# Optimization experiments

Hardware: AMD Instinct MI355X
Metric: run time of the kernel (lower is better)

The kernel has to match this reference:

```python
import jax, jax.numpy as jnp
import numpy as np

D_MODEL = 1024
NUM_HEADS = 16
HEAD_SIZE = D_MODEL // NUM_HEADS  # 64; used ONLY as the softmax scale (module never splits heads)


def setup_inputs() -> dict:
    key = jax.random.key(0)
    ks = jax.random.split(key, 7)
    B, L, D = 4, 2048, D_MODEL
    q = jax.random.normal(ks[0], (B, L, D), dtype=jnp.float32)
    k = jax.random.normal(ks[1], (B, L, D), dtype=jnp.float32)
    v = jax.random.normal(ks[2], (B, L, D), dtype=jnp.float32)
    s = 1.0 / np.sqrt(D)
    Wq = jax.random.uniform(ks[3], (D, D), jnp.float32, -s, s)
    Wk = jax.random.uniform(ks[4], (D, D), jnp.float32, -s, s)
    Wv = jax.random.uniform(ks[5], (D, D), jnp.float32, -s, s)
    Wproj = jax.random.uniform(ks[6], (D, D), jnp.float32, -s, s)
    return {"q": q, "k": k, "v": v, "Wq": Wq, "Wk": Wk, "Wv": Wv, "Wproj": Wproj}


def reference(q, k, v, Wq, Wk, Wv, Wproj):
    # nn.Linear(x) = x @ W.T; weights stored [out, in]
    L = q.shape[1]
    qh = jnp.einsum('bld,ed->ble', q, Wq)
    kh = jnp.einsum('bld,ed->ble', k, Wk)
    vh = jnp.einsum('bld,ed->ble', v, Wv)
    # NOTE: module attends over the full d_model channel (no head split),
    # but scales by head_size ** -0.5 — faithful to the source.
    att = jnp.einsum('bqd,bkd->bqk', qh, kh) * (HEAD_SIZE ** -0.5)
    causal = jnp.tril(jnp.ones((L, L), dtype=bool))  # bias buffer
    att = jnp.where(causal, att, -jnp.inf)
    att = jax.nn.softmax(att, axis=-1)
    y = jnp.einsum('bqk,bkd->bqd', att, vh)
    y = jnp.einsum('bld,ed->ble', y, Wproj)
    return y
```

## Files before the change

kernel.cpp:

```cpp
#include <hip/hip_runtime.h>
#include <hip/hip_bf16.h>
#include <stdint.h>

typedef __bf16 bf16x8 __attribute__((ext_vector_type(8)));
typedef float  f32x4  __attribute__((ext_vector_type(4)));
typedef unsigned short ushort8v __attribute__((ext_vector_type(8)));

__device__ __forceinline__ unsigned short f2bf(float f) {
  unsigned int u = __float_as_uint(f);
  u += 0x7FFF + ((u >> 16) & 1);
  return (unsigned short)(u >> 16);
}
__device__ __forceinline__ float bf2f(unsigned short h) {
  return __uint_as_float(((unsigned int)h) << 16);
}

#define GLOAD_LDS(gptr, ldsptr)                                                     \
  __builtin_amdgcn_global_load_lds(                                                 \
      (const __attribute__((address_space(1))) unsigned int*)(gptr),                \
      (__attribute__((address_space(3))) unsigned int*)(ldsptr), 16, 0, 0)

__global__ __launch_bounds__(512, 1) void gemm8p(
    const unsigned short* __restrict__ A,
    const unsigned short* __restrict__ B,
    unsigned short* __restrict__ C,
    int M, int N, int K, int ntn)
{
  const int nwg = gridDim.x, orig = blockIdx.x;
  const int qq = nwg >> 3, rr = nwg & 7, xcd = orig & 7, oo = orig >> 3;
  const int wg = (xcd < rr ? xcd * (qq + 1) : rr * (qq + 1) + (xcd - rr) * qq) + oo;
  const int mt = wg / ntn, nt = wg % ntn;

  __shared__ __align__(16) unsigned short lds[65536];

  const int tid  = threadIdx.x;
  const int wave = tid >> 6;
  const int lane = tid & 63;
  const int wr = wave >> 2, wc = wave & 3;
  const int li = lane & 15;
  const int rslot = (((lane >> 4) ^ ((lane >> 1) & 3)) << 4);

  f32x4 acc[8][4];
#pragma unroll
  for (int i = 0; i < 8; ++i)
#pragma unroll
    for (int j = 0; j < 4; ++j) acc[i][j] = (f32x4){0.f, 0.f, 0.f, 0.f};

  const int nkt = K / 64;

  const int srow = tid >> 2;
  const long scol = (long)(((tid & 3) ^ ((tid >> 3) & 3)) << 3);
  const long aoff0 = (long)(mt * 256 + srow) * K + scol;
  const long aoff1 = (long)(mt * 256 + 128 + srow) * K + scol;
  const long boff0 = (long)(nt * 256 + srow) * K + scol;
  const long boff1 = (long)(nt * 256 + 128 + srow) * K + scol;
  const int stw = wave * 1024;

#define AB(c, kh) (((c) * 2 + (kh)) * 16384)
#define BB(c, kh) (65536 + ((c) * 2 + (kh)) * 16384)
#define STAGE_A(c, kh, jt) do { const long o_ = (long)(jt) * 64 + (kh) * 32;        \
    GLOAD_LDS(A + aoff0 + o_, (char*)lds + AB(c, kh) + stw);                        \
    GLOAD_LDS(A + aoff1 + o_, (char*)lds + AB(c, kh) + 8192 + stw); } while (0)
#define STAGE_B(c, kh, jt) do { const long o_ = (long)(jt) * 64 + (kh) * 32;        \
    GLOAD_LDS(B + boff0 + o_, (char*)lds + BB(c, kh) + stw);                        \
    GLOAD_LDS(B + boff1 + o_, (char*)lds + BB(c, kh) + 8192 + stw); } while (0)
#define RD_A(c, kk, ms, mf) \
  (*(const bf16x8*)((const char*)lds + AB(c, kk) + (wr * 128 + (ms) * 64 + (mf) * 16 + li) * 64 + rslot))
#define RD_B(c, kk, nf) \
  (*(const bf16x8*)((const char*)lds + BB(c, kk) + (wc * 64 + (nf) * 16 + li) * 64 + rslot))
#define MM(msb, bb) do {                                                            \
    _Pragma("unroll")                                                               \
    for (int mf_ = 0; mf_ < 4; ++mf_)                                               \
    _Pragma("unroll")                                                               \
      for (int nf_ = 0; nf_ < 4; ++nf_)                                             \
        acc[(msb) + mf_][nf_] = __builtin_amdgcn_mfma_f32_16x16x32_bf16(            \
            a[mf_], bb[nf_], acc[(msb) + mf_][nf_], 0, 0, 0); } while (0)
#define LGKM0_FENCE do {                                                            \
    asm volatile("s_waitcnt lgkmcnt(0)" ::: "memory");                              \
    __builtin_amdgcn_sched_barrier(0); } while (0)
#define BARRIER do { __builtin_amdgcn_s_barrier();                                  \
    asm volatile("" ::: "memory"); } while (0)

  STAGE_A(0, 0, 0); STAGE_B(0, 0, 0); STAGE_A(0, 1, 0); STAGE_B(0, 1, 0);
  asm volatile("s_waitcnt vmcnt(0)" ::: "memory");
  BARRIER;

  bf16x8 a[4], b0[4], b1[4];
  for (int j = 0; j < nkt; ++j) {
    const int c = j & 1;
    const bool more = (j + 1 < nkt);

#pragma unroll
    for (int nf = 0; nf < 4; ++nf) b0[nf] = RD_B(c, 0, nf);
#pragma unroll
    for (int mf = 0; mf < 4; ++mf) a[mf] = RD_A(c, 0, 0, mf);
    if (more) STAGE_A(c ^ 1, 0, j + 1);
    BARRIER;
    LGKM0_FENCE;
    __builtin_amdgcn_s_setprio(1);
    MM(0, b0);
    __builtin_amdgcn_s_setprio(0);
    BARRIER;

#pragma unroll
    for (int mf = 0; mf < 4; ++mf) a[mf] = RD_A(c, 0, 1, mf);
    if (more) STAGE_B(c ^ 1, 0, j + 1);
    BARRIER;
    LGKM0_FENCE;
    __builtin_amdgcn_s_setprio(1);
    MM(4, b0);
    __builtin_amdgcn_s_setprio(0);
    asm volatile("s_waitcnt vmcnt(4)" ::: "memory");
    BARRIER;

#pragma unroll
    for (int nf = 0; nf < 4; ++nf) b1[nf] = RD_B(c, 1, nf);
#pragma unroll
    for (int mf = 0; mf < 4; ++mf) a[mf] = RD_A(c, 1, 0, mf);
    if (more) STAGE_A(c ^ 1, 1, j + 1);
    BARRIER;
    LGKM0_FENCE;
    __builtin_amdgcn_s_setprio(1);
    MM(0, b1);
    __builtin_amdgcn_s_setprio(0);
    BARRIER;

#pragma unroll
    for (int mf = 0; mf < 4; ++mf) a[mf] = RD_A(c, 1, 1, mf);
    if (more) STAGE_B(c ^ 1, 1, j + 1);
    BARRIER;
    LGKM0_FENCE;
    __builtin_amdgcn_s_setprio(1);
    MM(4, b1);
    __builtin_amdgcn_s_setprio(0);
    asm volatile("s_waitcnt vmcnt(4)" ::: "memory");
    BARRIER;
  }
#undef AB
#undef BB
#undef STAGE_A
#undef STAGE_B
#undef RD_A
#undef RD_B
#undef MM
#undef LGKM0_FENCE
#undef BARRIER

  const int rb = mt * 256 + wr * 128;
  const int cb = nt * 256 + wc * 64;
#pragma unroll
  for (int mi = 0; mi < 8; ++mi)
#pragma unroll
    for (int ni = 0; ni < 4; ++ni) {
      const int row0 = rb + mi * 16 + ((lane >> 4) << 2);
      const int col  = cb + ni * 16 + (lane & 15);
#pragma unroll
      for (int jj = 0; jj < 4; ++jj)
        C[(long)(row0 + jj) * N + col] = f2bf(acc[mi][ni][jj]);
    }
}

#define BM 128
#define BN 128
#define BK 32

__global__ __launch_bounds__(256, 3) void gemm_bt(
    const unsigned short* __restrict__ A,
    const unsigned short* __restrict__ B,
    void* __restrict__ C,
    int M, int N, int K, int ntiles,
    long sAz, long sBz, long sCz,
    int mode, int tilemap, float scale)
{
  int mt, nt;
  const int orig = blockIdx.x;
  if (tilemap == 0) {
    const int nwg = gridDim.x;
    const int qq = nwg >> 3, rr = nwg & 7, xc = orig & 7, oo = orig >> 3;
    const int wg = (xc < rr ? xc * (qq + 1) : rr * (qq + 1) + (xc - rr) * qq) + oo;
    mt = wg / ntiles; nt = wg % ntiles;
  } else if (tilemap == 1) {
    mt = (int)((sqrtf(8.f * orig + 1.f) - 1.f) * 0.5f);
    int base = mt * (mt + 1) / 2;
    if (orig < base) { mt--; base = mt * (mt + 1) / 2; }
    else if (orig >= base + mt + 1) { mt++; base = mt * (mt + 1) / 2; }
    nt = orig - base;
  } else {
    const int c = orig & 15;
    mt = (c & 8) ? (15 - (c & 7)) : c;
    nt = orig >> 4;
  }
  const int z = blockIdx.y;
  const int emode = (mode == 3) ? (z == 2 ? 1 : 0) : mode;

  A += sAz * (long)z;
  B += sBz * (long)z;

  __shared__ __align__(16) unsigned short As[3][BM * BK];
  __shared__ __align__(16) unsigned short Bs[3][BN * BK];

  const int tid  = threadIdx.x;
  const int wave = tid >> 6;
  const int lane = tid & 63;
  const int wr = wave >> 1, wc = wave & 1;

  f32x4 acc[4][4];
#pragma unroll
  for (int i = 0; i < 4; ++i)
#pragma unroll
    for (int j = 0; j < 4; ++j) acc[i][j] = (f32x4){0.f, 0.f, 0.f, 0.f};

  int kiters = K / BK;
  if (tilemap == 2) { const int kl = (mt + 1) * (BM / BK); if (kl < kiters) kiters = kl; }

  const int r0 = tid >> 2, s0 = tid & 3;
  const int c0 = ((s0 ^ ((r0 >> 1) & 3)) << 3);
  const int r1 = r0 + 64;
  const int c1 = ((s0 ^ ((r1 >> 1) & 3)) << 3);
  const long aoff0 = (long)(mt * BM + r0) * K + c0;
  const long aoff1 = (long)(mt * BM + r1) * K + c1;
  const long boff0 = (long)(nt * BN + r0) * K + c0;
  const long boff1 = (long)(nt * BN + r1) * K + c1;
  const unsigned ldsw = wave * 1024;

#define STAGE(bi, k0)                                                     \
  do {                                                                    \
    GLOAD_LDS(A + aoff0 + (k0), (char*)&As[bi][0]    + ldsw);             \
    GLOAD_LDS(A + aoff1 + (k0), (char*)&As[bi][2048] + ldsw);             \
    GLOAD_LDS(B + boff0 + (k0), (char*)&Bs[bi][0]    + ldsw);             \
    GLOAD_LDS(B + boff1 + (k0), (char*)&Bs[bi][2048] + ldsw);             \
  } while (0)

  STAGE(0, 0);
  if (kiters > 1) STAGE(1, BK);

  int cur = 0;
  for (int kt = 0; kt < kiters; ++kt) {
    const int rem = kiters - 1 - kt;
    if (rem >= 2) {
      int sb = cur + 2; if (sb >= 3) sb -= 3;
      STAGE(sb, (kt + 2) * BK);
      asm volatile("s_waitcnt vmcnt(8)" ::: "memory");
    } else if (rem == 1) {
      asm volatile("s_waitcnt vmcnt(4)" ::: "memory");
    } else {
      asm volatile("s_waitcnt vmcnt(0)" ::: "memory");
    }
    __builtin_amdgcn_s_barrier();
    asm volatile("" ::: "memory");

    bf16x8 af[4], bfr[4];
#pragma unroll
    for (int i = 0; i < 4; ++i) {
      const int ar = wr * 64 + i * 16 + (lane & 15);
      const int as = ((lane >> 4) ^ ((ar >> 1) & 3)) << 3;
      af[i] = *(const bf16x8*)&As[cur][ar * BK + as];
      const int br = wc * 64 + i * 16 + (lane & 15);
      const int bs = ((lane >> 4) ^ ((br >> 1) & 3)) << 3;
      bfr[i] = *(const bf16x8*)&Bs[cur][br * BK + bs];
    }
#pragma unroll
    for (int mi = 0; mi < 4; ++mi)
#pragma unroll
      for (int ni = 0; ni < 4; ++ni)
        acc[mi][ni] = __builtin_amdgcn_mfma_f32_16x16x32_bf16(af[mi], bfr[ni], acc[mi][ni], 0, 0, 0);

    asm volatile("" ::: "memory");
    __builtin_amdgcn_s_barrier();
    cur = (cur == 2) ? 0 : cur + 1;
  }
#undef STAGE

  const int rb = mt * BM + wr * 64;
  const int cb = nt * BN + wc * 64;

  if (emode == 0) {
    unsigned short* Cb = (unsigned short*)C + sCz * (long)z;
#pragma unroll
    for (int mi = 0; mi < 4; ++mi)
#pragma unroll
      for (int ni = 0; ni < 4; ++ni) {
        const int row0 = rb + mi * 16 + ((lane >> 4) << 2);
        const int col  = cb + ni * 16 + (lane & 15);
#pragma unroll
        for (int j = 0; j < 4; ++j)
          Cb[(long)(row0 + j) * N + col] = f2bf(acc[mi][ni][j] * scale);
      }
  } else if (emode == 1) {
    unsigned short* Cb = (unsigned short*)C + sCz * (long)z;
#pragma unroll
    for (int mi = 0; mi < 4; ++mi)
#pragma unroll
      for (int ni = 0; ni < 4; ++ni) {
        const int row0 = rb + mi * 16 + ((lane >> 4) << 2);
        const int col  = cb + ni * 16 + (lane & 15);
#pragma unroll
        for (int j = 0; j < 4; ++j) {
          const int row = row0 + j;
          const int b = row >> 11, l = row & 2047;
          Cb[((long)b * N + col) * 2048 + l] = f2bf(acc[mi][ni][j]);
        }
      }
  } else {
    float* Cf = (float*)C + sCz * (long)z;
#pragma unroll
    for (int mi = 0; mi < 4; ++mi)
#pragma unroll
      for (int ni = 0; ni < 4; ++ni) {
        const int row0 = rb + mi * 16 + ((lane >> 4) << 2);
        const int col  = cb + ni * 16 + (lane & 15);
#pragma unroll
        for (int j = 0; j < 4; ++j)
          Cf[(long)(row0 + j) * N + col] = acc[mi][ni][j] * scale;
      }
  }
}

__global__ __launch_bounds__(256) void softmax_causal(
    const unsigned short* __restrict__ S, unsigned short* __restrict__ P)
{
  const int r = blockIdx.x;
  const int b = r >> 11, q = r & 2047;
  const unsigned short* srow = S + ((long)b * 2048 + q) * 2048;
  unsigned short* prow = P + ((long)b * 2048 + q) * 2048;
  const int len = q + 1;
  const int lenceil = ((q >> 7) + 1) << 7;
  const int tid = threadIdx.x, lane = tid & 63, wave = tid >> 6;
  const int base = tid * 8;
  const bool active = base < lenceil;
  __shared__ float red[8];

  float vv[8];
#pragma unroll
  for (int i = 0; i < 8; ++i) vv[i] = -3.4e38f;
  if (active) {
    ushort8v xv = *(const ushort8v*)(srow + base);
#pragma unroll
    for (int i = 0; i < 8; ++i) vv[i] = bf2f(xv[i]);
  }

  float m = -3.4e38f;
#pragma unroll
  for (int i = 0; i < 8; ++i) if (base + i < len) m = fmaxf(m, vv[i]);
#pragma unroll
  for (int o = 32; o; o >>= 1) m = fmaxf(m, __shfl_xor(m, o));
  if (lane == 0) red[wave] = m;
  __syncthreads();
  m = fmaxf(fmaxf(red[0], red[1]), fmaxf(red[2], red[3]));

  float p[8], s = 0.f;
#pragma unroll
  for (int i = 0; i < 8; ++i) {
    p[i] = (base + i < len) ? __expf(vv[i] - m) : 0.f;
    s += p[i];
  }
#pragma unroll
  for (int o = 32; o; o >>= 1) s += __shfl_xor(s, o);
  if (lane == 0) red[4 + wave] = s;
  __syncthreads();
  s = (red[4] + red[5]) + (red[6] + red[7]);
  const float inv = 1.f / s;

  if (active) {
    ushort8v o16;
#pragma unroll
    for (int i = 0; i < 8; ++i) o16[i] = f2bf(p[i] * inv);
    *(ushort8v*)(prow + base) = o16;
  }
}

__global__ __launch_bounds__(256) void convert_all(
    const float* __restrict__ q, const float* __restrict__ k, const float* __restrict__ v,
    const float* __restrict__ wq, const float* __restrict__ wk,
    const float* __restrict__ wv, const float* __restrict__ wp,
    unsigned short* __restrict__ qkv, unsigned short* __restrict__ wb)
{
  const long NQ = 8192L * 1024 / 4;
  const long NW = 1024L * 1024 / 4;
  const int blk = blockIdx.x;
  const float* src; unsigned short* dst; long n; int nb, bb;
  if (blk < 1536) {
    const int s = blk >> 9;
    src = (s == 0) ? q : (s == 1) ? k : v;
    dst = qkv + (long)s * (8192L * 1024);
    n = NQ; nb = 512; bb = blk & 511;
  } else {
    const int s = (blk - 1536) >> 6;
    src = (s == 0) ? wq : (s == 1) ? wk : (s == 2) ? wv : wp;
    dst = wb + (long)s * (1024L * 1024);
    n = NW; nb = 64; bb = (blk - 1536) & 63;
  }
  for (long i = (long)bb * 256 + threadIdx.x; i < n; i += (long)nb * 256) {
    float4 x = ((const float4*)src)[i];
    ushort4 o;
    o.x = f2bf(x.x); o.y = f2bf(x.y); o.z = f2bf(x.z); o.w = f2bf(x.w);
    ((ushort4*)dst)[i] = o;
  }
}

extern "C" void kernel_launch(void* const* d_in, const int* in_sizes, int n_in,
                              void* d_out, int out_size, void* d_ws, size_t ws_size,
                              hipStream_t stream) {
  const float* q  = (const float*)d_in[0];
  const float* k  = (const float*)d_in[1];
  const float* v  = (const float*)d_in[2];
  const float* Wq = (const float*)d_in[3];
  const float* Wk = (const float*)d_in[4];
  const float* Wv = (const float*)d_in[5];
  const float* Wp = (const float*)d_in[6];
  float* out = (float*)d_out;

  const long D  = 1024;
  const long L  = 2048;
  const long ND = 8192 * D;
  const long NS = 4L * L * L;

  char* ws = (char*)d_ws;
  unsigned short* qh    = (unsigned short*)ws;
  unsigned short* kh    = qh  + ND;
  unsigned short* vhT   = kh  + ND;
  unsigned short* wbf   = vhT + ND;
  unsigned short* S     = wbf + 4L * D * D;
  unsigned short* qkvbf = S   + NS;
  unsigned short* P     = qkvbf;
  unsigned short* ybf   = P + NS;

  convert_all<<<1792, 256, 0, stream>>>(q, k, v, Wq, Wk, Wv, Wp, qkvbf, wbf);

  gemm8p<<<128, 512, 0, stream>>>(qkvbf, wbf, S, 8192, 1024, 1024, 4);

  gemm_bt<<<dim3(512, 3), 256, 0, stream>>>(qkvbf, wbf, qh,
      8192, 1024, 1024, 8, ND, D * D, ND, 3, 0, 1.0f);

  gemm_bt<<<dim3(136, 4), 256, 0, stream>>>(qh, kh, S,
      2048, 2048, 1024, 16, L * D, L * D, L * L, 0, 1, 0.125f);

  softmax_causal<<<8192, 256, 0, stream>>>(S, P);

  gemm_bt<<<dim3(128, 4), 256, 0, stream>>>(P, vhT, ybf,
      2048, 1024, 2048, 8, L * L, D * L, L * D, 0, 2, 1.0f);

  gemm_bt<<<dim3(512, 1), 256, 0, stream>>>(ybf, wbf + 3 * D * D, out,
      8192, 1024, 1024, 8, 0, 0, 0, 2, 0, 1.0f);
}
```

Before: 250.2 us.

## Route QKV projection and causal QK^T through 256x256 deep-prefetch GEMM kernel

Generalizes the 512-thread 256x256-tile gemm8p kernel with batch strides, epilogue modes, scale and a triangular tile map. The QKV projection and the causal QK^T now run on it instead of the 128x128 gemm_bt kernel. It also drops a stray gemm8p warm-up launch that wrote into S. The kernel's LDS prefetch is deepened so the next k-half is staged earlier, with adjusted vmcnt waits, to hide global load latency. Larger tiles cut redundant operand traffic, but occupancy is lower and the triangular grid has only 36 tiles per batch, which leaves some CUs idle and adds tail imbalance.

```diff
diff --git a/kernel.cpp b/kernel.cpp
--- a/kernel.cpp
+++ b/kernel.cpp
@@ -23,13 +23,29 @@
 __global__ __launch_bounds__(512, 1) void gemm8p(
     const unsigned short* __restrict__ A,
     const unsigned short* __restrict__ B,
-    unsigned short* __restrict__ C,
-    int M, int N, int K, int ntn)
+    void* __restrict__ C,
+    int M, int N, int K, int ntn,
+    long sAz, long sBz, long sCz,
+    int mode, int tilemap, float scale)
 {
-  const int nwg = gridDim.x, orig = blockIdx.x;
-  const int qq = nwg >> 3, rr = nwg & 7, xcd = orig & 7, oo = orig >> 3;
-  const int wg = (xcd < rr ? xcd * (qq + 1) : rr * (qq + 1) + (xcd - rr) * qq) + oo;
-  const int mt = wg / ntn, nt = wg % ntn;
+  int mt, nt;
+  const int orig = blockIdx.x;
+  if (tilemap == 0) {
+    const int nwg = gridDim.x;
+    const int qq = nwg >> 3, rr = nwg & 7, xcd = orig & 7, oo = orig >> 3;
+    const int wg = (xcd < rr ? xcd * (qq + 1) : rr * (qq + 1) + (xcd - rr) * qq) + oo;
+    mt = wg / ntn; nt = wg % ntn;
+  } else {
+    mt = (int)((sqrtf(8.f * orig + 1.f) - 1.f) * 0.5f);
+    int base = mt * (mt + 1) / 2;
+    if (orig < base) { mt--; base = mt * (mt + 1) / 2; }
+    else if (orig >= base + mt + 1) { mt++; base = mt * (mt + 1) / 2; }
+    nt = orig - base;
+  }
+  const int z = blockIdx.y;
+  const int emode = (mode == 3) ? (z == 2 ? 1 : 0) : mode;
+  A += sAz * (long)z;
+  B += sBz * (long)z;
 
   __shared__ __align__(16) unsigned short lds[65536];
 
@@ -82,19 +98,22 @@
     asm volatile("" ::: "memory"); } while (0)
 
   STAGE_A(0, 0, 0); STAGE_B(0, 0, 0); STAGE_A(0, 1, 0); STAGE_B(0, 1, 0);
-  asm volatile("s_waitcnt vmcnt(0)" ::: "memory");
+  if (nkt > 1) { STAGE_A(1, 0, 1); STAGE_B(1, 0, 1); }
+  if (nkt > 1) { asm volatile("s_waitcnt vmcnt(4)" ::: "memory"); }
+  else         { asm volatile("s_waitcnt vmcnt(0)" ::: "memory"); }
   BARRIER;
 
   bf16x8 a[4], b0[4], b1[4];
   for (int j = 0; j < nkt; ++j) {
     const int c = j & 1;
-    const bool more = (j + 1 < nkt);
+    const bool s1 = (j + 1 < nkt);
+    const bool s2 = (j + 2 < nkt);
 
 #pragma unroll
     for (int nf = 0; nf < 4; ++nf) b0[nf] = RD_B(c, 0, nf);
 #pragma unroll
     for (int mf = 0; mf < 4; ++mf) a[mf] = RD_A(c, 0, 0, mf);
-    if (more) STAGE_A(c ^ 1, 0, j + 1);
+    if (s1) STAGE_A(c ^ 1, 1, j + 1);
     BARRIER;
     LGKM0_FENCE;
     __builtin_amdgcn_s_setprio(1);
@@ -104,20 +123,21 @@
 
 #pragma unroll
     for (int mf = 0; mf < 4; ++mf) a[mf] = RD_A(c, 0, 1, mf);
-    if (more) STAGE_B(c ^ 1, 0, j + 1);
+    if (s1) STAGE_B(c ^ 1, 1, j + 1);
     BARRIER;
     LGKM0_FENCE;
     __builtin_amdgcn_s_setprio(1);
     MM(4, b0);
     __builtin_amdgcn_s_setprio(0);
-    asm volatile("s_waitcnt vmcnt(4)" ::: "memory");
+    if (s1) { asm volatile("s_waitcnt vmcnt(8)" ::: "memory"); }
+    else    { asm volatile("s_waitcnt vmcnt(0)" ::: "memory"); }
     BARRIER;
 
 #pragma unroll
     for (int nf = 0; nf < 4; ++nf) b1[nf] = RD_B(c, 1, nf);
 #pragma unroll
     for (int mf = 0; mf < 4; ++mf) a[mf] = RD_A(c, 1, 0, mf);
-    if (more) STAGE_A(c ^ 1, 1, j + 1);
+    if (s2) STAGE_A(c, 0, j + 2);
     BARRIER;
     LGKM0_FENCE;
     __builtin_amdgcn_s_setprio(1);
@@ -127,13 +147,14 @@
 
 #pragma unroll
     for (int mf = 0; mf < 4; ++mf) a[mf] = RD_A(c, 1, 1, mf);
-    if (more) STAGE_B(c ^ 1, 1, j + 1);
+    if (s2) STAGE_B(c, 0, j + 2);
     BARRIER;
     LGKM0_FENCE;
     __builtin_amdgcn_s_setprio(1);
     MM(4, b1);
     __builtin_amdgcn_s_setprio(0);
-    asm volatile("s_waitcnt vmcnt(4)" ::: "memory");
+    if (s2)      { asm volatile("s_waitcnt vmcnt(8)" ::: "memory"); }
+    else if (s1) { asm volatile("s_waitcnt vmcnt(4)" ::: "memory"); }
     BARRIER;
   }
 #undef AB
@@ -148,16 +169,34 @@
 
   const int rb = mt * 256 + wr * 128;
   const int cb = nt * 256 + wc * 64;
-#pragma unroll
-  for (int mi = 0; mi < 8; ++mi)
-#pragma unroll
-    for (int ni = 0; ni < 4; ++ni) {
-      const int row0 = rb + mi * 16 + ((lane >> 4) << 2);
-      const int col  = cb + ni * 16 + (lane & 15);
-#pragma unroll
-      for (int jj = 0; jj < 4; ++jj)
-        C[(long)(row0 + jj) * N + col] = f2bf(acc[mi][ni][jj]);
-    }
+  if (emode == 0) {
+    unsigned short* Cb = (unsigned short*)C + sCz * (long)z;
+#pragma unroll
+    for (int mi = 0; mi < 8; ++mi)
+#pragma unroll
+      for (int ni = 0; ni < 4; ++ni) {
+        const int row0 = rb + mi * 16 + ((lane >> 4) << 2);
+        const int col  = cb + ni * 16 + (lane & 15);
+#pragma unroll
+        for (int jj = 0; jj < 4; ++jj)
+          Cb[(long)(row0 + jj) * N + col] = f2bf(acc[mi][ni][jj] * scale);
+      }
+  } else {
+    unsigned short* Cb = (unsigned short*)C + sCz * (long)z;
+#pragma unroll
+    for (int mi = 0; mi < 8; ++mi)
+#pragma unroll
+      for (int ni = 0; ni < 4; ++ni) {
+        const int row0 = rb + mi * 16 + ((lane >> 4) << 2);
+        const int col  = cb + ni * 16 + (lane & 15);
+#pragma unroll
+        for (int jj = 0; jj < 4; ++jj) {
+          const int row = row0 + jj;
+          const int b = row >> 11, l = row & 2047;
+          Cb[((long)b * N + col) * 2048 + l] = f2bf(acc[mi][ni][jj]);
+        }
+      }
+  }
 }
 
 #define BM 128
@@ -179,19 +218,12 @@
     const int qq = nwg >> 3, rr = nwg & 7, xc = orig & 7, oo = orig >> 3;
     const int wg = (xc < rr ? xc * (qq + 1) : rr * (qq + 1) + (xc - rr) * qq) + oo;
     mt = wg / ntiles; nt = wg % ntiles;
-  } else if (tilemap == 1) {
-    mt = (int)((sqrtf(8.f * orig + 1.f) - 1.f) * 0.5f);
-    int base = mt * (mt + 1) / 2;
-    if (orig < base) { mt--; base = mt * (mt + 1) / 2; }
-    else if (orig >= base + mt + 1) { mt++; base = mt * (mt + 1) / 2; }
-    nt = orig - base;
   } else {
     const int c = orig & 15;
     mt = (c & 8) ? (15 - (c & 7)) : c;
     nt = orig >> 4;
   }
   const int z = blockIdx.y;
-  const int emode = (mode == 3) ? (z == 2 ? 1 : 0) : mode;
 
   A += sAz * (long)z;
   B += sBz * (long)z;
@@ -274,7 +306,7 @@
   const int rb = mt * BM + wr * 64;
   const int cb = nt * BN + wc * 64;
 
-  if (emode == 0) {
+  if (mode == 0) {
     unsigned short* Cb = (unsigned short*)C + sCz * (long)z;
 #pragma unroll
     for (int mi = 0; mi < 4; ++mi)
@@ -285,21 +317,6 @@
 #pragma unroll
         for (int j = 0; j < 4; ++j)
           Cb[(long)(row0 + j) * N + col] = f2bf(acc[mi][ni][j] * scale);
-      }
-  } else if (emode == 1) {
-    unsigned short* Cb = (unsigned short*)C + sCz * (long)z;
-#pragma unroll
-    for (int mi = 0; mi < 4; ++mi)
-#pragma unroll
-      for (int ni = 0; ni < 4; ++ni) {
-        const int row0 = rb + mi * 16 + ((lane >> 4) << 2);
-        const int col  = cb + ni * 16 + (lane & 15);
-#pragma unroll
-        for (int j = 0; j < 4; ++j) {
-          const int row = row0 + j;
-          const int b = row >> 11, l = row & 2047;
-          Cb[((long)b * N + col) * 2048 + l] = f2bf(acc[mi][ni][j]);
-        }
       }
   } else {
     float* Cf = (float*)C + sCz * (long)z;
@@ -427,13 +444,11 @@
 
   convert_all<<<1792, 256, 0, stream>>>(q, k, v, Wq, Wk, Wv, Wp, qkvbf, wbf);
 
-  gemm8p<<<128, 512, 0, stream>>>(qkvbf, wbf, S, 8192, 1024, 1024, 4);
-
-  gemm_bt<<<dim3(512, 3), 256, 0, stream>>>(qkvbf, wbf, qh,
-      8192, 1024, 1024, 8, ND, D * D, ND, 3, 0, 1.0f);
-
-  gemm_bt<<<dim3(136, 4), 256, 0, stream>>>(qh, kh, S,
-      2048, 2048, 1024, 16, L * D, L * D, L * L, 0, 1, 0.125f);
+  gemm8p<<<dim3(128, 3), 512, 0, stream>>>(qkvbf, wbf, qh,
+      8192, 1024, 1024, 4, ND, D * D, ND, 3, 0, 1.0f);
+
+  gemm8p<<<dim3(36, 4), 512, 0, stream>>>(qh, kh, S,
+      2048, 2048, 1024, 8, L * D, L * D, L * L, 0, 1, 0.125f);
 
   softmax_causal<<<8192, 256, 0, stream>>>(S, P);
 
```

Result: faster. 220.1 us (-12.0%).
